# Kernel tuning notes

Hardware: AMD Instinct MI355X
Metric: run time of the kernel (lower is better)

The kernel has to match this reference:

```python
import jax, jax.numpy as jnp
import numpy as np

C = 256  # channels
SHAPES = [(8, C, 80, 80), (8, C, 40, 40), (8, C, 20, 20), (8, C, 10, 10)]
EPS = 1e-8  # torch cosine_similarity eps


def _nearest_resize(x, H, W):
    # Matches F.interpolate(mode='nearest'): src_idx = floor(dst_idx * in/out)
    b, c, h, w = x.shape
    rows = (jnp.arange(H) * h) // H
    cols = (jnp.arange(W) * w) // W
    return x[:, :, rows[:, None], cols[None, :]]


def setup_inputs() -> dict:
    key = jax.random.key(0)
    ks = jax.random.split(key, 12)
    d = {}
    for i, s in enumerate(SHAPES):
        d[f"f{i}"] = jax.random.normal(ks[i], s, dtype=jnp.float32)
        d[f"w{i}"] = jax.random.normal(ks[4 + i], (C, C), dtype=jnp.float32) / jnp.sqrt(jnp.float32(C))
        d[f"b{i}"] = jax.random.normal(ks[8 + i], (C,), dtype=jnp.float32) * 0.01
    return d


def reference(f0, f1, f2, f3, w0, w1, w2, w3, b0, b1, b2, b3):
    feats = [f0, f1, f2, f3]
    ws = [w0, w1, w2, w3]
    bs = [b0, b1, b2, b3]
    H = max(f.shape[2] for f in feats)
    W = max(f.shape[3] for f in feats)
    proj = []
    for f, w, b in zip(feats, ws, bs):
        # 1x1 conv == per-pixel GEMM over channels
        p = jnp.einsum('bchw,oc->bohw', f, w) + b[None, :, None, None]
        if p.shape[2] != H or p.shape[3] != W:
            p = _nearest_resize(p, H, W)
        proj.append(p)
    B = proj[0].shape[0]
    N = len(proj)
    x = jnp.stack(proj, axis=1).reshape(B, N, C, H * W)  # [B,N,C,L]
    # Pairwise cosine similarity along channel dim at each spatial location,
    # then mean over locations (vectorized form of the O(N^2) torch loop).
    dot = jnp.einsum('bicl,bjcl->bijl', x, x)            # [B,N,N,L]
    nrm = jnp.sqrt(jnp.einsum('bicl,bicl->bil', x, x))   # [B,N,L]
    denom = jnp.maximum(nrm[:, :, None, :] * nrm[:, None, :, :], EPS)
    attn = (dot / denom).mean(axis=-1)                   # [B,N,N]
    return jax.nn.softmax(attn, axis=-1)
```

## Files before the change

kernel.cpp:

```cpp
#include <hip/hip_runtime.h>


#define CCH 256
#define WPITCH 40

typedef __attribute__((ext_vector_type(8))) short short8;
typedef __attribute__((ext_vector_type(4))) short short4_;
typedef __attribute__((ext_vector_type(4))) float float4_;

__device__ inline short f2bf(float x) {
    union { float f; unsigned u; } c; c.f = x;
    unsigned u = c.u + 0x7FFFu + ((c.u >> 16) & 1u);
    return (short)(u >> 16);
}
__device__ inline float bf2f(short b) {
    union { unsigned u; float f; } c; c.u = ((unsigned)(unsigned short)b) << 16;
    return c.f;
}

__global__ __launch_bounds__(256) void proj_norm(
    const float* __restrict__ f0, const float* __restrict__ f1,
    const float* __restrict__ f2, const float* __restrict__ f3,
    const float* __restrict__ w0, const float* __restrict__ w1,
    const float* __restrict__ w2, const float* __restrict__ w3,
    const float* __restrict__ b0, const float* __restrict__ b1,
    const float* __restrict__ b2, const float* __restrict__ b3,
    short* __restrict__ u0, short* __restrict__ u1,
    short* __restrict__ u2, short* __restrict__ u3)
{
    __shared__ __align__(16) short Wt[256 * WPITCH];
    __shared__ __align__(16) short Ft[64 * WPITCH];

    const int blk = blockIdx.x;
    int s, b, tile, L;
    const float* F; const float* Wg; const float* bias; short* U;
    if (blk < 800)       { s = 0; int r = blk;        b = r / 100; tile = r % 100; L = 6400; F = f0; Wg = w0; bias = b0; U = u0; }
    else if (blk < 1000) { s = 1; int r = blk - 800;  b = r / 25;  tile = r % 25;  L = 1600; F = f1; Wg = w1; bias = b1; U = u1; }
    else if (blk < 1056) { s = 2; int r = blk - 1000; b = r / 7;   tile = r % 7;   L = 400;  F = f2; Wg = w2; bias = b2; U = u2; }
    else                 { s = 3; int r = blk - 1056; b = r / 2;   tile = r % 2;   L = 100;  F = f3; Wg = w3; bias = b3; U = u3; }

    const int t    = threadIdx.x;
    const int lane = t & 63;
    const int wav  = t >> 6;
    const int ln   = lane & 15;
    const int quad = lane >> 4;
    const int pixbase = tile * 64;
    const float* Fb = F + (size_t)b * CCH * L;

    const int wo = t >> 2;
    const int wk = (t & 3) * 8;
    const int fpix = t & 63;
    const int fchunk = t >> 6;
    const int gpix0 = pixbase + fpix;
    const bool pin = gpix0 < L;
    const int gl0 = pin ? gpix0 : 0;

    float4_ wbufA[4], wbufB[4];
    float fbuf[8];

    auto loadW = [&](int ks) {
#pragma unroll
        for (int p = 0; p < 4; ++p) {
            const float* srcp = Wg + (size_t)(p * 64 + wo) * CCH + ks * 32 + wk;
            wbufA[p] = *(const float4_*)srcp;
            wbufB[p] = *(const float4_*)(srcp + 4);
        }
    };
    auto loadF = [&](int ks) {
        const float* fs = Fb + (size_t)(ks * 32 + fchunk * 8) * L + gl0;
#pragma unroll
        for (int j = 0; j < 8; ++j) fbuf[j] = fs[(size_t)j * L];
    };

    float4_ acc[16];
#pragma unroll
    for (int i = 0; i < 16; ++i) acc[i] = (float4_){0.f, 0.f, 0.f, 0.f};

    loadW(0);
    loadF(0);

    for (int ks = 0; ks < 8; ++ks) {
        __syncthreads();
#pragma unroll
        for (int p = 0; p < 4; ++p) {
            short8 v;
#pragma unroll
            for (int e = 0; e < 4; ++e) {
                v[e]     = f2bf(wbufA[p][e]);
                v[e + 4] = f2bf(wbufB[p][e]);
            }
            *(short8*)(&Wt[(p * 64 + wo) * WPITCH + wk]) = v;
        }
        {
            short8 v;
#pragma unroll
            for (int j = 0; j < 8; ++j) v[j] = pin ? f2bf(fbuf[j]) : (short)0;
            *(short8*)(&Ft[fpix * WPITCH + fchunk * 8]) = v;
        }
        __syncthreads();
        const int ksn = (ks + 1) & 7;
        loadW(ksn);
        loadF(ksn);

        short8 bfrag = *(const short8*)(&Ft[(wav * 16 + ln) * WPITCH + quad * 8]);
#pragma unroll
        for (int mt = 0; mt < 16; ++mt) {
            short8 afrag = *(const short8*)(&Wt[(mt * 16 + ln) * WPITCH + quad * 8]);
            acc[mt] = __builtin_amdgcn_mfma_f32_16x16x32_bf16(afrag, bfrag, acc[mt], 0, 0, 0);
        }
    }

    float ss = 0.f;
#pragma unroll
    for (int mt = 0; mt < 16; ++mt) {
        float4_ bv = *(const float4_*)(bias + mt * 16 + quad * 4);
#pragma unroll
        for (int r = 0; r < 4; ++r) {
            float v = acc[mt][r] + bv[r];
            acc[mt][r] = v;
            ss += v * v;
        }
    }
    ss += __shfl_xor(ss, 16);
    ss += __shfl_xor(ss, 32);
    const float inv = 1.f / sqrtf(fmaxf(ss, 1e-24f));

    const int gpixw = pixbase + wav * 16 + ln;
    if (gpixw < L) {
        short* dst = U + ((size_t)b * L + gpixw) * CCH;
#pragma unroll
        for (int mt = 0; mt < 16; ++mt) {
            short4_ v;
#pragma unroll
            for (int r = 0; r < 4; ++r) v[r] = f2bf(acc[mt][r] * inv);
            *(short4_*)(dst + mt * 16 + quad * 4) = v;
        }
    }
}

__global__ __launch_bounds__(256) void cell_dots(
    const short* __restrict__ u0, const short* __restrict__ u1,
    const short* __restrict__ u2, const short* __restrict__ u3,
    float* __restrict__ partial) {
    const int b  = blockIdx.y;
    const int c3 = blockIdx.x;
    const int H3 = c3 / 10, W3 = c3 - H3 * 10;
    const int t  = threadIdx.x;
    const int c1 = t >> 4;
    const int k  = t & 15;
    const int h1 = c1 >> 2, w1 = c1 & 3;
    const int r1 = 4 * H3 + h1, q1 = 4 * W3 + w1;
    const int px1 = r1 * 40 + q1;
    const int px2 = (2 * H3 + (h1 >> 1)) * 20 + (2 * W3 + (w1 >> 1));
    const int px3 = H3 * 10 + W3;

    float b1v[16], b2v[16], b3v[16];
    {
        const short* p1 = u1 + ((size_t)(b * 1600 + px1)) * CCH + k * 16;
        const short* p2 = u2 + ((size_t)(b * 400  + px2)) * CCH + k * 16;
        const short* p3 = u3 + ((size_t)(b * 100  + px3)) * CCH + k * 16;
#pragma unroll
        for (int h = 0; h < 2; ++h) {
            short8 v1 = *(const short8*)(p1 + h * 8);
            short8 v2 = *(const short8*)(p2 + h * 8);
            short8 v3 = *(const short8*)(p3 + h * 8);
#pragma unroll
            for (int e = 0; e < 8; ++e) {
                b1v[h * 8 + e] = bf2f(v1[e]);
                b2v[h * 8 + e] = bf2f(v2[e]);
                b3v[h * 8 + e] = bf2f(v3[e]);
            }
        }
    }

    float d01 = 0.f, d02 = 0.f, d03 = 0.f;
#pragma unroll
    for (int dh = 0; dh < 2; ++dh) {
#pragma unroll
        for (int dw = 0; dw < 2; ++dw) {
            const int px0 = (2 * r1 + dh) * 80 + 2 * q1 + dw;
            const short* pa = u0 + ((size_t)(b * 6400 + px0)) * CCH + k * 16;
            float av[16];
#pragma unroll
            for (int h = 0; h < 2; ++h) {
                short8 v = *(const short8*)(pa + h * 8);
#pragma unroll
                for (int e = 0; e < 8; ++e) av[h * 8 + e] = bf2f(v[e]);
            }
#pragma unroll
            for (int e = 0; e < 16; ++e) {
                d01 += av[e] * b1v[e];
                d02 += av[e] * b2v[e];
                d03 += av[e] * b3v[e];
            }
        }
    }
    float d12 = 0.f, d13 = 0.f, d23 = 0.f;
#pragma unroll
    for (int e = 0; e < 16; ++e) {
        d12 += b1v[e] * b2v[e];
        d13 += b1v[e] * b3v[e];
    }
    if (((h1 & 1) | (w1 & 1)) == 0) {
#pragma unroll
        for (int e = 0; e < 16; ++e) d23 += b2v[e] * b3v[e];
    }

    float vals[6] = {d01, d02, d03, d12, d13, d23};
    __shared__ float red[4][6];
    const int lane = t & 63, wav = t >> 6;
#pragma unroll
    for (int p = 0; p < 6; ++p) {
        float v = vals[p];
        v += __shfl_xor(v, 1);  v += __shfl_xor(v, 2);  v += __shfl_xor(v, 4);
        v += __shfl_xor(v, 8);  v += __shfl_xor(v, 16); v += __shfl_xor(v, 32);
        if (lane == 0) red[wav][p] = v;
    }
    __syncthreads();
    if (t < 6)
        partial[((size_t)b * 6 + t) * 100 + c3] =
            red[0][t] + red[1][t] + red[2][t] + red[3][t];
}

__global__ void softmax4(const float* __restrict__ partial, float* __restrict__ out) {
    int t = threadIdx.x;
    if (t >= 128) return;
    int b = t >> 4, i = (t >> 2) & 3, j = t & 3;
    float a[4];
#pragma unroll
    for (int jj = 0; jj < 4; ++jj) {
        if (jj == i) { a[jj] = 1.0f; continue; }
        int lo = i < jj ? i : jj;
        int hi = i < jj ? jj : i;
        int pidx;
        if (lo == 0) pidx = hi - 1;
        else if (lo == 1) pidx = 1 + hi;
        else pidx = 5;
        const float* pp = partial + ((size_t)b * 6 + pidx) * 100;
        float s = 0.f;
        for (int k = 0; k < 100; ++k) s += pp[k];
        int rf = 80 >> lo;
        a[jj] = s / (float)(rf * rf);
    }
    float m = fmaxf(fmaxf(a[0], a[1]), fmaxf(a[2], a[3]));
    float e0 = expf(a[0] - m), e1 = expf(a[1] - m), e2 = expf(a[2] - m), e3 = expf(a[3] - m);
    float sum = e0 + e1 + e2 + e3;
    float ev = (j == 0) ? e0 : (j == 1) ? e1 : (j == 2) ? e2 : e3;
    out[t] = ev / sum;
}

extern "C" void kernel_launch(void* const* d_in, const int* in_sizes, int n_in,
                              void* d_out, int out_size, void* d_ws, size_t ws_size,
                              hipStream_t stream) {
    const float* f[4]  = {(const float*)d_in[0], (const float*)d_in[3],
                          (const float*)d_in[6], (const float*)d_in[9]};
    const float* w[4]  = {(const float*)d_in[1], (const float*)d_in[4],
                          (const float*)d_in[7], (const float*)d_in[10]};
    const float* bs[4] = {(const float*)d_in[2], (const float*)d_in[5],
                          (const float*)d_in[8], (const float*)d_in[11]};

    const int Ls[4] = {6400, 1600, 400, 100};
    char* ws = (char*)d_ws;
    size_t off = 0;
    short* u[4];
    for (int s = 0; s < 4; ++s) {
        u[s] = (short*)(ws + off);
        off += (size_t)8 * CCH * Ls[s] * sizeof(short);
    }
    float* partial = (float*)(ws + off);

    proj_norm<<<1072, 256, 0, stream>>>(f[0], f[1], f[2], f[3],
                                        w[0], w[1], w[2], w[3],
                                        bs[0], bs[1], bs[2], bs[3],
                                        u[0], u[1], u[2], u[3]);

    cell_dots<<<dim3(100, 8), 256, 0, stream>>>(u[0], u[1], u[2], u[3], partial);

    softmax4<<<1, 128, 0, stream>>>(partial, (float*)d_out);
}
```

Before: 168.8 us.

## Fuse level-0 projection with cosine dot reduction, skipping u0 round trip

Splits the projection into one kernel for the three small levels and a new kernel that projects level 0 per 8x8 spatial cell and immediately computes the pairwise dots against the staged level-1/2/3 vectors held in shared memory. This removes writing and re-reading the largest normalized bf16 buffer (u0) through global memory. Each block now maps to a spatial 8x8 tile, so level-0 feature loads are strided rows of 8 pixels rather than 64 contiguous pixels. The whole level-0 GEMM must wait for the small-level kernel to finish.

```diff
diff --git a/kernel.cpp b/kernel.cpp
--- a/kernel.cpp
+++ b/kernel.cpp
@@ -18,26 +18,24 @@
     return c.f;
 }
 
-__global__ __launch_bounds__(256) void proj_norm(
-    const float* __restrict__ f0, const float* __restrict__ f1,
-    const float* __restrict__ f2, const float* __restrict__ f3,
-    const float* __restrict__ w0, const float* __restrict__ w1,
-    const float* __restrict__ w2, const float* __restrict__ w3,
-    const float* __restrict__ b0, const float* __restrict__ b1,
-    const float* __restrict__ b2, const float* __restrict__ b3,
-    short* __restrict__ u0, short* __restrict__ u1,
-    short* __restrict__ u2, short* __restrict__ u3)
+__global__ __launch_bounds__(256) void proj_small(
+    const float* __restrict__ f1, const float* __restrict__ f2,
+    const float* __restrict__ f3,
+    const float* __restrict__ w1, const float* __restrict__ w2,
+    const float* __restrict__ w3,
+    const float* __restrict__ b1, const float* __restrict__ b2,
+    const float* __restrict__ b3,
+    short* __restrict__ u1, short* __restrict__ u2, short* __restrict__ u3)
 {
     __shared__ __align__(16) short Wt[256 * WPITCH];
     __shared__ __align__(16) short Ft[64 * WPITCH];
 
     const int blk = blockIdx.x;
-    int s, b, tile, L;
+    int b, tile, L;
     const float* F; const float* Wg; const float* bias; short* U;
-    if (blk < 800)       { s = 0; int r = blk;        b = r / 100; tile = r % 100; L = 6400; F = f0; Wg = w0; bias = b0; U = u0; }
-    else if (blk < 1000) { s = 1; int r = blk - 800;  b = r / 25;  tile = r % 25;  L = 1600; F = f1; Wg = w1; bias = b1; U = u1; }
-    else if (blk < 1056) { s = 2; int r = blk - 1000; b = r / 7;   tile = r % 7;   L = 400;  F = f2; Wg = w2; bias = b2; U = u2; }
-    else                 { s = 3; int r = blk - 1056; b = r / 2;   tile = r % 2;   L = 100;  F = f3; Wg = w3; bias = b3; U = u3; }
+    if (blk < 200)      { int r = blk;       b = r / 25; tile = r % 25; L = 1600; F = f1; Wg = w1; bias = b1; U = u1; }
+    else if (blk < 256) { int r = blk - 200; b = r / 7;  tile = r % 7;  L = 400;  F = f2; Wg = w2; bias = b2; U = u2; }
+    else                { int r = blk - 256; b = r / 2;  tile = r % 2;  L = 100;  F = f3; Wg = w3; bias = b3; U = u3; }
 
     const int t    = threadIdx.x;
     const int lane = t & 63;
@@ -57,7 +55,6 @@
 
     float4_ wbufA[4], wbufB[4];
     float fbuf[8];
-
     auto loadW = [&](int ks) {
 #pragma unroll
         for (int p = 0; p < 4; ++p) {
@@ -76,19 +73,14 @@
 #pragma unroll
     for (int i = 0; i < 16; ++i) acc[i] = (float4_){0.f, 0.f, 0.f, 0.f};
 
-    loadW(0);
-    loadF(0);
-
+    loadW(0); loadF(0);
     for (int ks = 0; ks < 8; ++ks) {
         __syncthreads();
 #pragma unroll
         for (int p = 0; p < 4; ++p) {
             short8 v;
 #pragma unroll
-            for (int e = 0; e < 4; ++e) {
-                v[e]     = f2bf(wbufA[p][e]);
-                v[e + 4] = f2bf(wbufB[p][e]);
-            }
+            for (int e = 0; e < 4; ++e) { v[e] = f2bf(wbufA[p][e]); v[e + 4] = f2bf(wbufB[p][e]); }
             *(short8*)(&Wt[(p * 64 + wo) * WPITCH + wk]) = v;
         }
         {
@@ -99,8 +91,7 @@
         }
         __syncthreads();
         const int ksn = (ks + 1) & 7;
-        loadW(ksn);
-        loadF(ksn);
+        loadW(ksn); loadF(ksn);
 
         short8 bfrag = *(const short8*)(&Ft[(wav * 16 + ln) * WPITCH + quad * 8]);
 #pragma unroll
@@ -115,11 +106,7 @@
     for (int mt = 0; mt < 16; ++mt) {
         float4_ bv = *(const float4_*)(bias + mt * 16 + quad * 4);
 #pragma unroll
-        for (int r = 0; r < 4; ++r) {
-            float v = acc[mt][r] + bv[r];
-            acc[mt][r] = v;
-            ss += v * v;
-        }
+        for (int r = 0; r < 4; ++r) { float v = acc[mt][r] + bv[r]; acc[mt][r] = v; ss += v * v; }
     }
     ss += __shfl_xor(ss, 16);
     ss += __shfl_xor(ss, 32);
@@ -138,88 +125,191 @@
     }
 }
 
-__global__ __launch_bounds__(256) void cell_dots(
-    const short* __restrict__ u0, const short* __restrict__ u1,
-    const short* __restrict__ u2, const short* __restrict__ u3,
-    float* __restrict__ partial) {
+__global__ __launch_bounds__(256) void proj0_dots(
+    const float* __restrict__ F, const float* __restrict__ Wg,
+    const float* __restrict__ bias,
+    const short* __restrict__ u1, const short* __restrict__ u2,
+    const short* __restrict__ u3,
+    float* __restrict__ partial)
+{
+    __shared__ __align__(16) short Wt[256 * WPITCH];
+    __shared__ __align__(16) short Ft[64 * WPITCH];
+    short* S1 = Wt;
+    short* S2 = Wt + 4096;
+    short* S3 = Wt + 5120;
+    __shared__ float red[4][3];
+    __shared__ float redB[3];
+
+    const int c3 = blockIdx.x;
     const int b  = blockIdx.y;
-    const int c3 = blockIdx.x;
     const int H3 = c3 / 10, W3 = c3 - H3 * 10;
-    const int t  = threadIdx.x;
-    const int c1 = t >> 4;
-    const int k  = t & 15;
-    const int h1 = c1 >> 2, w1 = c1 & 3;
-    const int r1 = 4 * H3 + h1, q1 = 4 * W3 + w1;
-    const int px1 = r1 * 40 + q1;
-    const int px2 = (2 * H3 + (h1 >> 1)) * 20 + (2 * W3 + (w1 >> 1));
-    const int px3 = H3 * 10 + W3;
-
-    float b1v[16], b2v[16], b3v[16];
+
+    const int t    = threadIdx.x;
+    const int lane = t & 63;
+    const int wav  = t >> 6;
+    const int ln   = lane & 15;
+    const int quad = lane >> 4;
+    const float* Fb = F + (size_t)b * CCH * 6400;
+
+    const int wo = t >> 2;
+    const int wk = (t & 3) * 8;
+    const int fpix = t & 63;
+    const int fchunk = t >> 6;
+    const int gl = (8 * H3 + (fpix >> 3)) * 80 + 8 * W3 + (fpix & 7);
+
+    float4_ wbufA[4], wbufB[4];
+    float fbuf[8];
+    auto loadW = [&](int ks) {
+#pragma unroll
+        for (int p = 0; p < 4; ++p) {
+            const float* srcp = Wg + (size_t)(p * 64 + wo) * CCH + ks * 32 + wk;
+            wbufA[p] = *(const float4_*)srcp;
+            wbufB[p] = *(const float4_*)(srcp + 4);
+        }
+    };
+    auto loadF = [&](int ks) {
+        const float* fs = Fb + (size_t)(ks * 32 + fchunk * 8) * 6400 + gl;
+#pragma unroll
+        for (int j = 0; j < 8; ++j) fbuf[j] = fs[(size_t)j * 6400];
+    };
+
+    float4_ acc[16];
+#pragma unroll
+    for (int i = 0; i < 16; ++i) acc[i] = (float4_){0.f, 0.f, 0.f, 0.f};
+
+    loadW(0); loadF(0);
+    for (int ks = 0; ks < 8; ++ks) {
+        __syncthreads();
+#pragma unroll
+        for (int p = 0; p < 4; ++p) {
+            short8 v;
+#pragma unroll
+            for (int e = 0; e < 4; ++e) { v[e] = f2bf(wbufA[p][e]); v[e + 4] = f2bf(wbufB[p][e]); }
+            *(short8*)(&Wt[(p * 64 + wo) * WPITCH + wk]) = v;
+        }
+        {
+            short8 v;
+#pragma unroll
+            for (int j = 0; j < 8; ++j) v[j] = f2bf(fbuf[j]);
+            *(short8*)(&Ft[fpix * WPITCH + fchunk * 8]) = v;
+        }
+        __syncthreads();
+        const int ksn = (ks + 1) & 7;
+        loadW(ksn); loadF(ksn);
+
+        short8 bfrag = *(const short8*)(&Ft[(wav * 16 + ln) * WPITCH + quad * 8]);
+#pragma unroll
+        for (int mt = 0; mt < 16; ++mt) {
+            short8 afrag = *(const short8*)(&Wt[(mt * 16 + ln) * WPITCH + quad * 8]);
+            acc[mt] = __builtin_amdgcn_mfma_f32_16x16x32_bf16(afrag, bfrag, acc[mt], 0, 0, 0);
+        }
+    }
+
+    float ss = 0.f;
+#pragma unroll
+    for (int mt = 0; mt < 16; ++mt) {
+        float4_ bv = *(const float4_*)(bias + mt * 16 + quad * 4);
+#pragma unroll
+        for (int r = 0; r < 4; ++r) { float v = acc[mt][r] + bv[r]; acc[mt][r] = v; ss += v * v; }
+    }
+    ss += __shfl_xor(ss, 16);
+    ss += __shfl_xor(ss, 32);
+    const float inv = 1.f / sqrtf(fmaxf(ss, 1e-24f));
+
+    __syncthreads();
+
     {
-        const short* p1 = u1 + ((size_t)(b * 1600 + px1)) * CCH + k * 16;
-        const short* p2 = u2 + ((size_t)(b * 400  + px2)) * CCH + k * 16;
-        const short* p3 = u3 + ((size_t)(b * 100  + px3)) * CCH + k * 16;
-#pragma unroll
-        for (int h = 0; h < 2; ++h) {
-            short8 v1 = *(const short8*)(p1 + h * 8);
-            short8 v2 = *(const short8*)(p2 + h * 8);
-            short8 v3 = *(const short8*)(p3 + h * 8);
-#pragma unroll
-            for (int e = 0; e < 8; ++e) {
-                b1v[h * 8 + e] = bf2f(v1[e]);
-                b2v[h * 8 + e] = bf2f(v2[e]);
-                b3v[h * 8 + e] = bf2f(v3[e]);
-            }
-        }
-    }
-
+        const int p1 = t >> 4, ck = (t & 15) * 16;
+        const int h1 = p1 >> 2, w1 = p1 & 3;
+        const short* src = u1 + ((size_t)(b * 1600 + (4 * H3 + h1) * 40 + 4 * W3 + w1)) * CCH + ck;
+        *(short8*)(&S1[p1 * 256 + ck])     = *(const short8*)src;
+        *(short8*)(&S1[p1 * 256 + ck + 8]) = *(const short8*)(src + 8);
+    }
+    if (t < 64) {
+        const int p2 = t >> 4, ck = (t & 15) * 16;
+        const int h2 = p2 >> 1, w2 = p2 & 1;
+        const short* src = u2 + ((size_t)(b * 400 + (2 * H3 + h2) * 20 + 2 * W3 + w2)) * CCH + ck;
+        *(short8*)(&S2[p2 * 256 + ck])     = *(const short8*)src;
+        *(short8*)(&S2[p2 * 256 + ck + 8]) = *(const short8*)(src + 8);
+    }
+    if (t < 16) {
+        const int ck = t * 16;
+        const short* src = u3 + ((size_t)(b * 100 + H3 * 10 + W3)) * CCH + ck;
+        *(short8*)(&S3[ck])     = *(const short8*)src;
+        *(short8*)(&S3[ck + 8]) = *(const short8*)(src + 8);
+    }
+    __syncthreads();
+
+    const int pme = wav * 16 + ln;
+    const int ph = pme >> 3, pw = pme & 7;
+    const int c1 = (ph >> 1) * 4 + (pw >> 1);
+    const int c2 = (ph >> 2) * 2 + (pw >> 2);
     float d01 = 0.f, d02 = 0.f, d03 = 0.f;
 #pragma unroll
-    for (int dh = 0; dh < 2; ++dh) {
-#pragma unroll
-        for (int dw = 0; dw < 2; ++dw) {
-            const int px0 = (2 * r1 + dh) * 80 + 2 * q1 + dw;
-            const short* pa = u0 + ((size_t)(b * 6400 + px0)) * CCH + k * 16;
-            float av[16];
-#pragma unroll
-            for (int h = 0; h < 2; ++h) {
-                short8 v = *(const short8*)(pa + h * 8);
-#pragma unroll
-                for (int e = 0; e < 8; ++e) av[h * 8 + e] = bf2f(v[e]);
-            }
-#pragma unroll
-            for (int e = 0; e < 16; ++e) {
-                d01 += av[e] * b1v[e];
-                d02 += av[e] * b2v[e];
-                d03 += av[e] * b3v[e];
-            }
-        }
-    }
-    float d12 = 0.f, d13 = 0.f, d23 = 0.f;
-#pragma unroll
-    for (int e = 0; e < 16; ++e) {
-        d12 += b1v[e] * b2v[e];
-        d13 += b1v[e] * b3v[e];
-    }
-    if (((h1 & 1) | (w1 & 1)) == 0) {
-#pragma unroll
-        for (int e = 0; e < 16; ++e) d23 += b2v[e] * b3v[e];
-    }
-
-    float vals[6] = {d01, d02, d03, d12, d13, d23};
-    __shared__ float red[4][6];
-    const int lane = t & 63, wav = t >> 6;
-#pragma unroll
-    for (int p = 0; p < 6; ++p) {
+    for (int mt = 0; mt < 16; ++mt) {
+        const int ch = mt * 16 + quad * 4;
+        short4_ v1 = *(const short4_*)(&S1[c1 * 256 + ch]);
+        short4_ v2 = *(const short4_*)(&S2[c2 * 256 + ch]);
+        short4_ v3 = *(const short4_*)(&S3[ch]);
+#pragma unroll
+        for (int r = 0; r < 4; ++r) {
+            float a = acc[mt][r] * inv;
+            d01 += a * bf2f(v1[r]);
+            d02 += a * bf2f(v2[r]);
+            d03 += a * bf2f(v3[r]);
+        }
+    }
+    float vals[3] = {d01, d02, d03};
+#pragma unroll
+    for (int p = 0; p < 3; ++p) {
         float v = vals[p];
         v += __shfl_xor(v, 1);  v += __shfl_xor(v, 2);  v += __shfl_xor(v, 4);
         v += __shfl_xor(v, 8);  v += __shfl_xor(v, 16); v += __shfl_xor(v, 32);
         if (lane == 0) red[wav][p] = v;
     }
+
+    if (wav == 0) {
+        float e12 = 0.f, e13 = 0.f, e23 = 0.f;
+        {
+            const int cc1 = lane >> 2, q = lane & 3;
+            const int cc2 = ((cc1 >> 2) >> 1) * 2 + ((cc1 & 3) >> 1);
+#pragma unroll
+            for (int k = 0; k < 16; ++k) {
+                short4_ a1 = *(const short4_*)(&S1[cc1 * 256 + q * 64 + k * 4]);
+                short4_ a2 = *(const short4_*)(&S2[cc2 * 256 + q * 64 + k * 4]);
+                short4_ a3 = *(const short4_*)(&S3[q * 64 + k * 4]);
+#pragma unroll
+                for (int r = 0; r < 4; ++r) {
+                    float x1 = bf2f(a1[r]);
+                    e12 += x1 * bf2f(a2[r]);
+                    e13 += x1 * bf2f(a3[r]);
+                }
+            }
+        }
+        if (lane < 16) {
+            const int dc2 = lane >> 2, dq = lane & 3;
+#pragma unroll
+            for (int k = 0; k < 16; ++k) {
+                short4_ a2 = *(const short4_*)(&S2[dc2 * 256 + dq * 64 + k * 4]);
+                short4_ a3 = *(const short4_*)(&S3[dq * 64 + k * 4]);
+#pragma unroll
+                for (int r = 0; r < 4; ++r) e23 += bf2f(a2[r]) * bf2f(a3[r]);
+            }
+        }
+        float evals[3] = {e12, e13, e23};
+#pragma unroll
+        for (int p = 0; p < 3; ++p) {
+            float v = evals[p];
+            v += __shfl_xor(v, 1);  v += __shfl_xor(v, 2);  v += __shfl_xor(v, 4);
+            v += __shfl_xor(v, 8);  v += __shfl_xor(v, 16); v += __shfl_xor(v, 32);
+            if (lane == 0) redB[p] = v;
+        }
+    }
     __syncthreads();
-    if (t < 6)
-        partial[((size_t)b * 6 + t) * 100 + c3] =
-            red[0][t] + red[1][t] + red[2][t] + red[3][t];
+    if (t < 3)
+        partial[((size_t)b * 6 + t) * 100 + c3] = red[0][t] + red[1][t] + red[2][t] + red[3][t];
+    else if (t < 6)
+        partial[((size_t)b * 6 + t) * 100 + c3] = redB[t - 3];
 }
 
 __global__ void softmax4(const float* __restrict__ partial, float* __restrict__ out) {
@@ -259,22 +349,20 @@
     const float* bs[4] = {(const float*)d_in[2], (const float*)d_in[5],
                           (const float*)d_in[8], (const float*)d_in[11]};
 
-    const int Ls[4] = {6400, 1600, 400, 100};
     char* ws = (char*)d_ws;
     size_t off = 0;
-    short* u[4];
-    for (int s = 0; s < 4; ++s) {
-        u[s] = (short*)(ws + off);
-        off += (size_t)8 * CCH * Ls[s] * sizeof(short);
-    }
+    short* u1 = (short*)(ws + off); off += (size_t)8 * CCH * 1600 * sizeof(short);
+    short* u2 = (short*)(ws + off); off += (size_t)8 * CCH * 400  * sizeof(short);
+    short* u3 = (short*)(ws + off); off += (size_t)8 * CCH * 100  * sizeof(short);
     float* partial = (float*)(ws + off);
 
-    proj_norm<<<1072, 256, 0, stream>>>(f[0], f[1], f[2], f[3],
-                                        w[0], w[1], w[2], w[3],
-                                        bs[0], bs[1], bs[2], bs[3],
-                                        u[0], u[1], u[2], u[3]);
-
-    cell_dots<<<dim3(100, 8), 256, 0, stream>>>(u[0], u[1], u[2], u[3], partial);
+    proj_small<<<272, 256, 0, stream>>>(f[1], f[2], f[3],
+                                        w[1], w[2], w[3],
+                                        bs[1], bs[2], bs[3],
+                                        u1, u2, u3);
+
+    proj0_dots<<<dim3(100, 8), 256, 0, stream>>>(f[0], w[0], bs[0],
+                                                 u1, u2, u3, partial);
 
     softmax4<<<1, 128, 0, stream>>>(partial, (float*)d_out);
 }
```

Result: no change. 167.7 us (-0.7%).
